# Kernel tuning notes

Hardware: AMD Instinct MI355X
Metric: run time of the kernel (lower is better)

Reference implementation:

```python
import jax, jax.numpy as jnp
import numpy as np
import math

HEAD_NUM = 16


def _split_qkv(qkv, head_num):
    # torch: rearrange(qkv, 'b t (d k h) -> k b h t d', k=3, h=head_num)
    B, T, E3 = qkv.shape
    d = E3 // (3 * head_num)
    qkv = qkv.reshape(B, T, d, 3, head_num)        # (b,t,d,k,h)
    qkv = jnp.transpose(qkv, (3, 0, 4, 1, 2))       # (k,b,h,t,d)
    return qkv[0], qkv[1], qkv[2]


def setup_inputs() -> dict:
    key = jax.random.key(0)
    ks = jax.random.split(key, 6)
    B, T, E = 4, 1024, 1024
    return {
        "x": jax.random.normal(ks[0], (B, T, E), dtype=jnp.float32),
        "y": jax.random.normal(ks[1], (B, T, E), dtype=jnp.float32),
        "Wqkv1": jax.random.normal(ks[2], (3 * E, E), dtype=jnp.float32) * 0.02,
        "Wqkv2": jax.random.normal(ks[3], (3 * E, E), dtype=jnp.float32) * 0.02,
        "Wout1": jax.random.normal(ks[4], (E, E), dtype=jnp.float32) * 0.02,
        "Wout2": jax.random.normal(ks[5], (E, E), dtype=jnp.float32) * 0.02,
    }


def reference(x, y, Wqkv1, Wqkv2, Wout1, Wout2):
    B, T, E = x.shape
    H = HEAD_NUM
    dk = math.sqrt(E / H)

    qkv1 = x @ Wqkv1.T                              # (B,T,3E)
    qkv2 = y @ Wqkv2.T
    q1, k1, v1 = _split_qkv(qkv1, H)                # each (B,H,T,d)
    q2, k2, v2 = _split_qkv(qkv2, H)

    # cross attention: stream-2 queries attend to stream-1 keys/values and vice versa
    energy1 = jnp.einsum('bhid,bhjd->bhij', q2, k1) / dk
    energy2 = jnp.einsum('bhid,bhjd->bhij', q1, k2) / dk
    attn1 = jax.nn.softmax(energy1, axis=-1)
    attn2 = jax.nn.softmax(energy2, axis=-1)

    xo = jnp.einsum('bhij,bhjd->bhid', attn1, v1)   # (B,H,T,d)
    yo = jnp.einsum('bhij,bhjd->bhid', attn2, v2)
    xo = jnp.transpose(xo, (0, 2, 1, 3)).reshape(B, T, E)  # b t (h d)
    yo = jnp.transpose(yo, (0, 2, 1, 3)).reshape(B, T, E)

    return xo @ Wout1.T, yo @ Wout2.T
```

## Files before the change

### kernel.cpp

```cpp
#include <hip/hip_runtime.h>
#include <hip/hip_bf16.h>

typedef __hip_bfloat16 bf16;
typedef __attribute__((ext_vector_type(8))) short short8;
typedef __attribute__((ext_vector_type(4))) short short4v;
typedef __attribute__((ext_vector_type(4))) float f32x4;

#define MFMA_BF16(a, b, c) __builtin_amdgcn_mfma_f32_16x16x32_bf16((a), (b), (c), 0, 0, 0)

#define QSCALE 0.1803368860111270f

__device__ __forceinline__ short f2bf(float f) {
    union { bf16 h; short s; } u;
    u.h = __float2bfloat16(f);
    return u.s;
}

#if defined(__has_builtin) && __has_builtin(__builtin_amdgcn_cvt_pk_bf16_f32)
typedef __attribute__((ext_vector_type(2))) __bf16 bf16x2_t;
__device__ __forceinline__ unsigned int pk2(float a, float b) {
    union { bf16x2_t v; unsigned int u; } x;
    x.v = __builtin_amdgcn_cvt_pk_bf16_f32(a, b);
    return x.u;
}
#else
__device__ __forceinline__ unsigned int pk2(float a, float b) {
    union { bf16 h[2]; unsigned int u; } x;
    x.h[0] = __float2bfloat16(a);
    x.h[1] = __float2bfloat16(b);
    return x.u;
}
#endif

__device__ __forceinline__ void gload16(const void* g, void* l) {
    __builtin_amdgcn_global_load_lds(
        (const __attribute__((address_space(1))) unsigned int*)g,
        (__attribute__((address_space(3))) unsigned int*)l, 16, 0, 0);
}

__global__ void cvt_fused(const float* __restrict__ x, const float* __restrict__ y,
                          const float* __restrict__ wo1, const float* __restrict__ wo2,
                          const float* __restrict__ wq1, const float* __restrict__ wq2,
                          bf16* __restrict__ ox, bf16* __restrict__ oy,
                          bf16* __restrict__ oo1, bf16* __restrict__ oo2,
                          bf16* __restrict__ oq1, bf16* __restrict__ oq2) {
    const int yb = blockIdx.y;
    if (yb < 4) {
        int i = blockIdx.x * 256 + threadIdx.x;
        const float* src; bf16* dst; int n4;
        switch (yb) {
            case 0:  src = x;   dst = ox;  n4 = 1048576; break;
            case 1:  src = y;   dst = oy;  n4 = 1048576; break;
            case 2:  src = wo1; dst = oo1; n4 = 262144;  break;
            default: src = wo2; dst = oo2; n4 = 262144;  break;
        }
        if (i >= n4) return;
        float4 f = reinterpret_cast<const float4*>(src)[i];
        short4v s;
        s.x = f2bf(f.x); s.y = f2bf(f.y); s.z = f2bf(f.z); s.w = f2bf(f.w);
        reinterpret_cast<short4v*>(dst)[i] = s;
    } else {
        const int np = blockIdx.x;
        if (np >= 3072) return;
        const int comp = np >> 10, rem = np & 1023, h = rem >> 6, d = rem & 63;
        const int srow = d * 48 + comp * 16 + h;
        const float* src = ((yb == 5) ? wq2 : wq1) + (long)srow * 1024;
        bf16* dst = ((yb == 5) ? oq2 : oq1) + (long)np * 1024;
        const float sc = (comp == 0) ? QSCALE : 1.0f;
        int t = threadIdx.x;
        float4 f = reinterpret_cast<const float4*>(src)[t];
        short4v s;
        s.x = f2bf(f.x * sc); s.y = f2bf(f.y * sc); s.z = f2bf(f.z * sc); s.w = f2bf(f.w * sc);
        reinterpret_cast<short4v*>(dst)[t] = s;
    }
}

template <int MODE>
__global__ __launch_bounds__(256)
void gemm_k(const bf16* __restrict__ A0g, const bf16* __restrict__ B0g,
            void* o0a, void* o0b, void* o0c,
            const bf16* __restrict__ A1g, const bf16* __restrict__ B1g,
            void* o1a, void* o1b, void* o1c, int N) {
    __shared__ short smem[20480];
    const int z = blockIdx.z;
    const short* A = reinterpret_cast<const short*>(z ? A1g : A0g);
    const short* B = reinterpret_cast<const short*>(z ? B1g : B0g);
    const int tid  = threadIdx.x;
    const int lane = tid & 63;
    const int w    = tid >> 6;
    const int wr   = w >> 1;
    const int wc   = w & 1;
    const int quad = lane >> 4;
    const int l16  = lane & 15;
    const long bM = (long)blockIdx.y * 128;

    f32x4 acc[4][4] = {};

    const int sr  = lane >> 2;
    const int scs = ((lane & 3) ^ (sr & 3)) * 8;
    const short* Ag0 = A + (bM + 32 * w + sr) * 1024 + scs;
    const short* Ag1 = Ag0 + 16 * 1024;
    const short* Bg0 = B + ((long)blockIdx.x * 128 + 32 * w + sr) * 1024 + scs;
    const short* Bg1 = Bg0 + 16 * 1024;

    const int sq = (quad ^ (l16 & 3)) * 8;

    {
        short* sb = smem;
        gload16(Ag0, sb + w * 1024);
        gload16(Ag1, sb + w * 1024 + 512);
        gload16(Bg0, sb + 4096 + w * 1024);
        gload16(Bg1, sb + 4096 + w * 1024 + 512);
    }
    __syncthreads();

    for (int iter = 0; iter < 32; ++iter) {
        const int cur = iter & 1;
        if (iter < 31) {
            const int koff = (iter + 1) * 32;
            short* sb = smem + (cur ^ 1) * 8192;
            gload16(Ag0 + koff, sb + w * 1024);
            gload16(Ag1 + koff, sb + w * 1024 + 512);
            gload16(Bg0 + koff, sb + 4096 + w * 1024);
            gload16(Bg1 + koff, sb + 4096 + w * 1024 + 512);
        }
        const short* Ab = smem + cur * 8192;
        const short* Bb = Ab + 4096;

        short8 af[4], bfr[4];
#pragma unroll
        for (int mt = 0; mt < 4; ++mt)
            af[mt] = *reinterpret_cast<const short8*>(&Ab[(wr * 64 + mt * 16 + l16) * 32 + sq]);
#pragma unroll
        for (int nt = 0; nt < 4; ++nt)
            bfr[nt] = *reinterpret_cast<const short8*>(&Bb[(wc * 64 + nt * 16 + l16) * 32 + sq]);
#pragma unroll
        for (int mt = 0; mt < 4; ++mt)
#pragma unroll
            for (int nt = 0; nt < 4; ++nt)
                acc[mt][nt] = MFMA_BF16(af[mt], bfr[nt], acc[mt][nt]);

        __syncthreads();
    }

    if (MODE == 1) {
        float* C = reinterpret_cast<float*>(z ? o1a : o0a);
        const long crow = bM + wr * 64 + quad * 4;
        const long ccol = (long)blockIdx.x * 128 + wc * 64 + l16;
#pragma unroll
        for (int mt = 0; mt < 4; ++mt)
#pragma unroll
            for (int nt = 0; nt < 4; ++nt)
#pragma unroll
                for (int r = 0; r < 4; ++r)
                    C[(crow + mt * 16 + r) * (long)N + ccol + nt * 16] = acc[mt][nt][r];
        return;
    }

    if (blockIdx.x < 16) {
        short* dst = reinterpret_cast<short*>(blockIdx.x >= 8 ? (z ? o1b : o0b)
                                                              : (z ? o1a : o0a));
        const int hd0 = (int)(blockIdx.x & 7) * 128 + wc * 64;
        const int b = (int)(bM >> 10);
        const int t0 = ((int)bM & 1023) + wr * 64 + quad * 4;
#pragma unroll
        for (int nt = 0; nt < 4; ++nt) {
            const int hd = hd0 + nt * 16 + l16;
            const int h = hd >> 6, d = hd & 63;
            short* dp = dst + ((long)(b * 16 + h) * 1024) * 64 + d;
#pragma unroll
            for (int mt = 0; mt < 4; ++mt)
#pragma unroll
                for (int r = 0; r < 4; ++r)
                    dp[(long)(t0 + mt * 16 + r) * 64] = f2bf(acc[mt][nt][r]);
        }
    } else {
        short* vT = reinterpret_cast<short*>(z ? o1c : o0c);
        const int h = ((int)blockIdx.x - 16) * 2 + wc;
        const int b = (int)(bM >> 10);
        const int tb = ((int)bM & 1023) + wr * 64;
        short* ws = smem + w * 4608;
#pragma unroll
        for (int nt = 0; nt < 4; ++nt)
#pragma unroll
            for (int mt = 0; mt < 4; ++mt) {
                uint2 uu;
                uu.x = pk2(acc[mt][nt][0], acc[mt][nt][1]);
                uu.y = pk2(acc[mt][nt][2], acc[mt][nt][3]);
                *reinterpret_cast<uint2*>(&ws[(nt * 16 + l16) * 72 + mt * 16 + quad * 4]) = uu;
            }
        short* vbase = vT + (long)(b * 16 + h) * 64 * 1024;
#pragma unroll
        for (int p = 0; p < 8; ++p) {
            const int d = p * 8 + (lane >> 3);
            const int ch = (lane & 7) * 8;
            short8 v = *reinterpret_cast<const short8*>(&ws[d * 72 + ch]);
            *reinterpret_cast<short8*>(&vbase[(long)d * 1024 + tb + ch]) = v;
        }
    }
}

__global__ __launch_bounds__(256)
void attn_kernel(const bf16* __restrict__ q0g, const bf16* __restrict__ k0g,
                 const bf16* __restrict__ v0g, bf16* __restrict__ o0g,
                 const bf16* __restrict__ q1g, const bf16* __restrict__ k1g,
                 const bf16* __restrict__ v1g, bf16* __restrict__ o1g) {
    __shared__ short smem[16384];
    const int bh = blockIdx.x;
    const int qt = blockIdx.y;
    const int z = blockIdx.z;
    const int b = bh >> 4, h = bh & 15;
    const int tid = threadIdx.x, lane = tid & 63, w = tid >> 6;
    const int quad = lane >> 4, l16 = lane & 15;

    const short* Qb = reinterpret_cast<const short*>(z ? q1g : q0g) + (long)bh * 1024 * 64;
    const short* Kb = reinterpret_cast<const short*>(z ? k1g : k0g) + (long)bh * 1024 * 64;
    const short* Vb = reinterpret_cast<const short*>(z ? v1g : v0g) + (long)bh * 64 * 1024;
    short* Ob = reinterpret_cast<short*>(z ? o1g : o0g);

    short8 qb[2][2];
#pragma unroll
    for (int qg = 0; qg < 2; ++qg) {
        const short* Qp = Qb + (long)(qt * 128 + qg * 64 + w * 16 + l16) * 64;
        qb[qg][0] = *reinterpret_cast<const short8*>(Qp + quad * 8);
        qb[qg][1] = *reinterpret_cast<const short8*>(Qp + 32 + quad * 8);
    }

    const int r8  = lane >> 3;
    const int sc8 = ((lane & 7) ^ r8) * 8;
    const short* Kg0 = Kb + (long)(16 * w + r8) * 64 + sc8;
    const short* Kg1 = Kg0 + 8 * 64;
    const short* Vg0 = Vb + (long)(16 * w + r8) * 1024 + sc8;
    const short* Vg1 = Vg0 + 8 * 1024;

    const int jbase = 8 * (l16 >> 2) + (l16 & 3);

    f32x4 o[2][4] = {};
    float li[2] = {0.f, 0.f};

    {
        short* sb = smem;
        gload16(Kg0, sb + w * 1024);
        gload16(Kg1, sb + w * 1024 + 512);
        gload16(Vg0, sb + 4096 + w * 1024);
        gload16(Vg1, sb + 4096 + w * 1024 + 512);
    }
    __syncthreads();

    for (int iter = 0; iter < 16; ++iter) {
        const int cur = iter & 1;
        if (iter < 15) {
            const long ko = (long)(iter + 1) * 4096;
            const long vo = (long)(iter + 1) * 64;
            short* sb = smem + (cur ^ 1) * 8192;
            gload16(Kg0 + ko, sb + w * 1024);
            gload16(Kg1 + ko, sb + w * 1024 + 512);
            gload16(Vg0 + vo, sb + 4096 + w * 1024);
            gload16(Vg1 + vo, sb + 4096 + w * 1024 + 512);
        }
        const short* Ks = smem + cur * 8192;
        const short* Vs = Ks + 4096;

        f32x4 st[2][4];
#pragma unroll
        for (int g = 0; g < 4; ++g) {
            const int goff = (g >> 1) * 32 + (g & 1) * 4;
            const int row = jbase + goff;
            const int s0 = (quad ^ (row & 7)) * 8;
            const short* kr = Ks + row * 64;
            short8 k0 = *reinterpret_cast<const short8*>(kr + s0);
            short8 k1 = *reinterpret_cast<const short8*>(kr + (s0 ^ 32));
#pragma unroll
            for (int qg = 0; qg < 2; ++qg) {
                f32x4 zf = {0.f, 0.f, 0.f, 0.f};
                zf = MFMA_BF16(k0, qb[qg][0], zf);
                zf = MFMA_BF16(k1, qb[qg][1], zf);
                st[qg][g] = zf;
            }
        }

        union { unsigned int u[4]; short8 s; } f0[2], f1[2];
#pragma unroll
        for (int qg = 0; qg < 2; ++qg) {
            float p[4][4];
            float rs = 0.f;
#pragma unroll
            for (int g = 0; g < 4; ++g)
#pragma unroll
                for (int r = 0; r < 4; ++r) {
                    float e = exp2f(st[qg][g][r]);
                    p[g][r] = e;
                    rs += e;
                }
            li[qg] += rs;
            f0[qg].u[0] = pk2(p[0][0], p[0][1]); f0[qg].u[1] = pk2(p[0][2], p[0][3]);
            f0[qg].u[2] = pk2(p[1][0], p[1][1]); f0[qg].u[3] = pk2(p[1][2], p[1][3]);
            f1[qg].u[0] = pk2(p[2][0], p[2][1]); f1[qg].u[1] = pk2(p[2][2], p[2][3]);
            f1[qg].u[2] = pk2(p[3][0], p[3][1]); f1[qg].u[3] = pk2(p[3][2], p[3][3]);
        }

#pragma unroll
        for (int dt = 0; dt < 4; ++dt) {
            const int rv = dt * 16 + l16;
            const int sv = (quad ^ (rv & 7)) * 8;
            const short* vr = Vs + rv * 64;
            short8 v0 = *reinterpret_cast<const short8*>(vr + sv);
            short8 v1 = *reinterpret_cast<const short8*>(vr + (sv ^ 32));
#pragma unroll
            for (int qg = 0; qg < 2; ++qg) {
                o[qg][dt] = MFMA_BF16(v0, f0[qg].s, o[qg][dt]);
                o[qg][dt] = MFMA_BF16(v1, f1[qg].s, o[qg][dt]);
            }
        }

        __syncthreads();
    }

#pragma unroll
    for (int qg = 0; qg < 2; ++qg) {
        li[qg] += __shfl_xor(li[qg], 16);
        li[qg] += __shfl_xor(li[qg], 32);
    }

#pragma unroll
    for (int qg = 0; qg < 2; ++qg) {
        short* Os = smem + qg * 5120 + w * 1280;
        const float rl = 1.0f / li[qg];
#pragma unroll
        for (int dt = 0; dt < 4; ++dt) {
            uint2 uu;
            uu.x = pk2(o[qg][dt][0] * rl, o[qg][dt][1] * rl);
            uu.y = pk2(o[qg][dt][2] * rl, o[qg][dt][3] * rl);
            *reinterpret_cast<uint2*>(&Os[l16 * 80 + dt * 16 + quad * 4]) = uu;
        }
#pragma unroll
        for (int p = 0; p < 2; ++p) {
            int row = p * 8 + (lane >> 3);
            int ch = (lane & 7) * 8;
            short8 v = *reinterpret_cast<const short8*>(&Os[row * 80 + ch]);
            *reinterpret_cast<short8*>(&Ob[((long)(b * 1024) + qt * 128 + qg * 64 + w * 16 + row) * 1024 + h * 64 + ch]) = v;
        }
    }
}

extern "C" void kernel_launch(void* const* d_in, const int* in_sizes, int n_in,
                              void* d_out, int out_size, void* d_ws, size_t ws_size,
                              hipStream_t stream) {
    const float* x     = (const float*)d_in[0];
    const float* y     = (const float*)d_in[1];
    const float* Wqkv1 = (const float*)d_in[2];
    const float* Wqkv2 = (const float*)d_in[3];
    const float* Wout1 = (const float*)d_in[4];
    const float* Wout2 = (const float*)d_in[5];

    char* ws = (char*)d_ws;
    bf16* Wqkv1b = (bf16*)(ws + 0);
    bf16* Wqkv2b = (bf16*)(ws + 6291456);
    bf16* Wout1b = (bf16*)(ws + 12582912);
    bf16* Wout2b = (bf16*)(ws + 14680064);
    bf16* xb     = (bf16*)(ws + 16777216);
    bf16* yb     = (bf16*)(ws + 25165824);
    bf16* q1     = (bf16*)(ws + 33554432);
    bf16* k1     = (bf16*)(ws + 41943040);
    bf16* v1T    = (bf16*)(ws + 50331648);
    bf16* q2     = (bf16*)(ws + 58720256);
    bf16* k2     = (bf16*)(ws + 67108864);
    bf16* v2T    = (bf16*)(ws + 75497472);
    bf16* xo     = xb;
    bf16* yo     = yb;

    cvt_fused<<<dim3(4096, 6), 256, 0, stream>>>(x, y, Wout1, Wout2, Wqkv1, Wqkv2,
                                                 xb, yb, Wout1b, Wout2b, Wqkv1b, Wqkv2b);

    gemm_k<0><<<dim3(24, 32, 2), 256, 0, stream>>>(xb, Wqkv1b, q1, k1, v1T,
                                                   yb, Wqkv2b, q2, k2, v2T, 3072);

    attn_kernel<<<dim3(64, 8, 2), 256, 0, stream>>>(q2, k1, v1T, xo,
                                                    q1, k2, v2T, yo);

    gemm_k<1><<<dim3(8, 32, 2), 256, 0, stream>>>(xo, Wout1b, (float*)d_out, nullptr, nullptr,
                                                  yo, Wout2b, ((float*)d_out) + 4194304, nullptr, nullptr,
                                                  1024);
}
```

Baseline: 264.2 us.

## Add 256x256 QKV GEMM with staged async loads and pipeline attention K/V loads

Replaces the 128x128 QKV projection GEMM with a 512-thread 256x256-tile kernel. It uses 128KB of dynamic LDS double-buffered across four sub-phases, vmcnt-gated barriers, and setprio around MFMA bursts to overlap global loads with compute. The attention kernel now splits K and V prefetches so V loads are issued after the QK MFMAs, and it waits on partial vmcnt instead of full syncthreads. It also changes the swizzle patterns. The aim is to raise data reuse per tile and hide load latency, at the cost of heavier register and LDS use that limits occupancy, plus hand-tuned waitcnt counts that are fragile.

After: 263.9 us. No clear change (-0.1%).

```diff
diff --git a/kernel.cpp b/kernel.cpp
--- a/kernel.cpp
+++ b/kernel.cpp
@@ -75,13 +75,168 @@
     }
 }
 
+#define GATE4 do { asm volatile("s_waitcnt vmcnt(4)" ::: "memory"); \
+    __builtin_amdgcn_s_barrier(); __builtin_amdgcn_sched_barrier(0); } while (0)
+
+__global__ __launch_bounds__(512, 2)
+void gemm_qkv256(const bf16* __restrict__ A0g, const bf16* __restrict__ B0g,
+                 void* o0a, void* o0b, void* o0c,
+                 const bf16* __restrict__ A1g, const bf16* __restrict__ B1g,
+                 void* o1a, void* o1b, void* o1c) {
+    extern __shared__ short smem[];
+    const int z = blockIdx.z;
+    const short* A = reinterpret_cast<const short*>(z ? A1g : A0g);
+    const short* B = reinterpret_cast<const short*>(z ? B1g : B0g);
+    const int tid  = threadIdx.x;
+    const int lane = tid & 63;
+    const int w    = tid >> 6;
+    const int quad = lane >> 4;
+    const int l16  = lane & 15;
+    const long M0 = (long)blockIdx.y * 256;
+    const long N0 = (long)blockIdx.x * 256;
+
+    const int rowblk = (w >> 2) * 64;
+    const int colblk = (w & 3) * 32;
+    const int cA0  = (quad ^ (l16 & 7)) * 8;
+    const int aoff = (rowblk + l16) * 64;
+    const int boff = 16384 + (colblk + l16) * 64;
+    const int w512 = w * 512;
+
+    const short* Asrc = A + (M0 + w * 8 + (lane >> 3)) * 1024 + ((lane & 7) ^ (lane >> 3)) * 8;
+    const short* Bsrc = B + (N0 + w * 8 + (lane >> 3)) * 1024 + ((lane & 7) ^ (lane >> 3)) * 8;
+
+    f32x4 acc[4][4][2] = {};
+    short8 af[4][2], bfv[2][2];
+
+#define SA256(half, tt, nbase) do { \
+    const short* _s = Asrc + (half) * 131072 + (tt) * 64; \
+    short* _d = smem + (nbase) + (half) * 8192 + w512; \
+    gload16(_s, _d); gload16(_s + 65536, _d + 4096); } while (0)
+#define SB256(half, tt, nbase) do { \
+    const short* _s = Bsrc + (half) * 131072 + (tt) * 64; \
+    short* _d = smem + (nbase) + 16384 + (half) * 8192 + w512; \
+    gload16(_s, _d); gload16(_s + 65536, _d + 4096); } while (0)
+#define RDA256(Ah, bbv) do { \
+    _Pragma("unroll") for (int mt = 0; mt < 4; ++mt) { \
+        const short* _p = &smem[(bbv) + (Ah) * 8192 + aoff + mt * 1024]; \
+        af[mt][0] = *reinterpret_cast<const short8*>(_p + cA0); \
+        af[mt][1] = *reinterpret_cast<const short8*>(_p + (cA0 ^ 32)); } } while (0)
+#define RDB256(Bh, bbv) do { \
+    _Pragma("unroll") for (int nt = 0; nt < 2; ++nt) { \
+        const short* _p = &smem[(bbv) + (Bh) * 8192 + boff + nt * 1024]; \
+        bfv[nt][0] = *reinterpret_cast<const short8*>(_p + cA0); \
+        bfv[nt][1] = *reinterpret_cast<const short8*>(_p + (cA0 ^ 32)); } } while (0)
+#define MM256(p) do { \
+    __builtin_amdgcn_s_setprio(1); \
+    _Pragma("unroll") for (int mt = 0; mt < 4; ++mt) \
+    _Pragma("unroll") for (int nt = 0; nt < 2; ++nt) { \
+        acc[p][mt][nt] = MFMA_BF16(af[mt][0], bfv[nt][0], acc[p][mt][nt]); \
+        acc[p][mt][nt] = MFMA_BF16(af[mt][1], bfv[nt][1], acc[p][mt][nt]); } \
+    __builtin_amdgcn_s_setprio(0); } while (0)
+
+    SA256(0, 0, 0); SB256(0, 0, 0); SB256(1, 0, 0); SA256(1, 0, 0);
+
+#pragma unroll 1
+    for (int t = 0; t < 15; ++t) {
+        const int bb = (t & 1) << 15;
+        const int nb = bb ^ 32768;
+        GATE4;
+        SA256(0, t + 1, nb);
+        RDA256(0, bb); RDB256(0, bb);
+        __builtin_amdgcn_sched_barrier(0);
+        MM256(0);
+        GATE4;
+        SB256(0, t + 1, nb);
+        RDB256(1, bb);
+        __builtin_amdgcn_sched_barrier(0);
+        MM256(1);
+        GATE4;
+        SB256(1, t + 1, nb);
+        RDA256(1, bb); RDB256(0, bb);
+        __builtin_amdgcn_sched_barrier(0);
+        MM256(2);
+        SA256(1, t + 1, nb);
+        RDB256(1, bb);
+        __builtin_amdgcn_sched_barrier(0);
+        MM256(3);
+    }
+    asm volatile("s_waitcnt vmcnt(0)" ::: "memory");
+    __builtin_amdgcn_s_barrier();
+    __builtin_amdgcn_sched_barrier(0);
+    {
+        const int bb = 32768;
+        RDA256(0, bb); RDB256(0, bb); MM256(0);
+        RDB256(1, bb); MM256(1);
+        RDA256(1, bb); RDB256(0, bb); MM256(2);
+        RDB256(1, bb); MM256(3);
+    }
+
+    if (blockIdx.x < 8) {
+        short* dst = reinterpret_cast<short*>(blockIdx.x < 4 ? (z ? o1a : o0a)
+                                                             : (z ? o1b : o0b));
+        const int b = (int)(M0 >> 10);
+        const int t00 = ((int)M0 & 1023);
+        const int hd00 = ((int)blockIdx.x & 3) * 256;
+#pragma unroll
+        for (int p = 0; p < 4; ++p) {
+            const int Ah = p >> 1, Bh = p & 1;
+            const int tr0 = t00 + Ah * 128 + rowblk + quad * 4;
+#pragma unroll
+            for (int nt = 0; nt < 2; ++nt) {
+                const int hd = hd00 + Bh * 128 + colblk + nt * 16 + l16;
+                const int h = hd >> 6, d = hd & 63;
+                short* dp = dst + (long)(b * 16 + h) * 65536 + d;
+#pragma unroll
+                for (int mt = 0; mt < 4; ++mt)
+#pragma unroll
+                    for (int r = 0; r < 4; ++r)
+                        dp[(long)(tr0 + mt * 16 + r) * 64] = f2bf(acc[p][mt][nt][r]);
+            }
+        }
+    } else {
+        short* vT = reinterpret_cast<short*>(z ? o1c : o0c);
+        const int b = (int)(M0 >> 10);
+        const int hd00 = ((int)blockIdx.x - 8) * 256;
+        short* ws = smem + w * 2304;
+        const int c8 = (lane & 7) * 8;
+        const int colr = lane >> 3;
+#pragma unroll
+        for (int p = 0; p < 4; ++p) {
+            const int Ah = p >> 1, Bh = p & 1;
+#pragma unroll
+            for (int nt = 0; nt < 2; ++nt)
+#pragma unroll
+                for (int mt = 0; mt < 4; ++mt) {
+                    uint2 uu;
+                    uu.x = pk2(acc[p][mt][nt][0], acc[p][mt][nt][1]);
+                    uu.y = pk2(acc[p][mt][nt][2], acc[p][mt][nt][3]);
+                    *reinterpret_cast<uint2*>(&ws[(nt * 16 + l16) * 72 + mt * 16 + quad * 4]) = uu;
+                }
+            const int tb = ((int)M0 & 1023) + Ah * 128 + rowblk + c8;
+#pragma unroll
+            for (int q4 = 0; q4 < 4; ++q4) {
+                const int col = q4 * 8 + colr;
+                const int hd = hd00 + Bh * 128 + colblk + col;
+                const int h = hd >> 6, d = hd & 63;
+                short8 v = *reinterpret_cast<const short8*>(&ws[col * 72 + c8]);
+                *reinterpret_cast<short8*>(&vT[(long)(b * 16 + h) * 65536 + (long)d * 1024 + tb]) = v;
+            }
+        }
+    }
+#undef SA256
+#undef SB256
+#undef RDA256
+#undef RDB256
+#undef MM256
+}
+
 template <int MODE>
 __global__ __launch_bounds__(256)
 void gemm_k(const bf16* __restrict__ A0g, const bf16* __restrict__ B0g,
             void* o0a, void* o0b, void* o0c,
             const bf16* __restrict__ A1g, const bf16* __restrict__ B1g,
             void* o1a, void* o1b, void* o1c, int N) {
-    __shared__ short smem[20480];
+    __shared__ short smem2[20480];
     const int z = blockIdx.z;
     const short* A = reinterpret_cast<const short*>(z ? A1g : A0g);
     const short* B = reinterpret_cast<const short*>(z ? B1g : B0g);
@@ -102,11 +257,10 @@
     const short* Ag1 = Ag0 + 16 * 1024;
     const short* Bg0 = B + ((long)blockIdx.x * 128 + 32 * w + sr) * 1024 + scs;
     const short* Bg1 = Bg0 + 16 * 1024;
-
     const int sq = (quad ^ (l16 & 3)) * 8;
 
     {
-        short* sb = smem;
+        short* sb = smem2;
         gload16(Ag0, sb + w * 1024);
         gload16(Ag1, sb + w * 1024 + 512);
         gload16(Bg0, sb + 4096 + w * 1024);
@@ -118,13 +272,13 @@
         const int cur = iter & 1;
         if (iter < 31) {
             const int koff = (iter + 1) * 32;
-            short* sb = smem + (cur ^ 1) * 8192;
+            short* sb = smem2 + (cur ^ 1) * 8192;
             gload16(Ag0 + koff, sb + w * 1024);
             gload16(Ag1 + koff, sb + w * 1024 + 512);
             gload16(Bg0 + koff, sb + 4096 + w * 1024);
             gload16(Bg1 + koff, sb + 4096 + w * 1024 + 512);
         }
-        const short* Ab = smem + cur * 8192;
+        const short* Ab = smem2 + cur * 8192;
         const short* Bb = Ab + 4096;
 
         short8 af[4], bfr[4];
@@ -156,7 +310,6 @@
                     C[(crow + mt * 16 + r) * (long)N + ccol + nt * 16] = acc[mt][nt][r];
         return;
     }
-
     if (blockIdx.x < 16) {
         short* dst = reinterpret_cast<short*>(blockIdx.x >= 8 ? (z ? o1b : o0b)
                                                               : (z ? o1a : o0a));
@@ -173,29 +326,6 @@
 #pragma unroll
                 for (int r = 0; r < 4; ++r)
                     dp[(long)(t0 + mt * 16 + r) * 64] = f2bf(acc[mt][nt][r]);
-        }
-    } else {
-        short* vT = reinterpret_cast<short*>(z ? o1c : o0c);
-        const int h = ((int)blockIdx.x - 16) * 2 + wc;
-        const int b = (int)(bM >> 10);
-        const int tb = ((int)bM & 1023) + wr * 64;
-        short* ws = smem + w * 4608;
-#pragma unroll
-        for (int nt = 0; nt < 4; ++nt)
-#pragma unroll
-            for (int mt = 0; mt < 4; ++mt) {
-                uint2 uu;
-                uu.x = pk2(acc[mt][nt][0], acc[mt][nt][1]);
-                uu.y = pk2(acc[mt][nt][2], acc[mt][nt][3]);
-                *reinterpret_cast<uint2*>(&ws[(nt * 16 + l16) * 72 + mt * 16 + quad * 4]) = uu;
-            }
-        short* vbase = vT + (long)(b * 16 + h) * 64 * 1024;
-#pragma unroll
-        for (int p = 0; p < 8; ++p) {
-            const int d = p * 8 + (lane >> 3);
-            const int ch = (lane & 7) * 8;
-            short8 v = *reinterpret_cast<const short8*>(&ws[d * 72 + ch]);
-            *reinterpret_cast<short8*>(&vbase[(long)d * 1024 + tb + ch]) = v;
         }
     }
 }
@@ -227,47 +357,48 @@
     }
 
     const int r8  = lane >> 3;
-    const int sc8 = ((lane & 7) ^ r8) * 8;
-    const short* Kg0 = Kb + (long)(16 * w + r8) * 64 + sc8;
-    const short* Kg1 = Kg0 + 8 * 64;
-    const short* Vg0 = Vb + (long)(16 * w + r8) * 1024 + sc8;
-    const short* Vg1 = Vg0 + 8 * 1024;
+    const int sc0 = ((lane & 7) ^ (r8 & 3)) * 8;
+    const short* Kg0 = Kb + (long)(16 * w + r8) * 64 + sc0;
+    const short* Kg1 = Kb + (long)(16 * w + 8 + r8) * 64 + (sc0 ^ 32);
+    const short* Vg0 = Vb + (long)(16 * w + r8) * 1024 + sc0;
+    const short* Vg1 = Vb + (long)(16 * w + 8 + r8) * 1024 + (sc0 ^ 32);
 
     const int jbase = 8 * (l16 >> 2) + (l16 & 3);
+    const int fKs = (l16 & 3) | (((l16 >> 2) & 1) << 2);
+    const int s0  = (quad ^ fKs) * 8;
+    const int fVs = (l16 & 3) | (((l16 >> 3) & 1) << 2);
+    const int sv  = (quad ^ fVs) * 8;
 
     f32x4 o[2][4] = {};
     float li[2] = {0.f, 0.f};
 
-    {
-        short* sb = smem;
-        gload16(Kg0, sb + w * 1024);
-        gload16(Kg1, sb + w * 1024 + 512);
-        gload16(Vg0, sb + 4096 + w * 1024);
-        gload16(Vg1, sb + 4096 + w * 1024 + 512);
-    }
-    __syncthreads();
-
+    gload16(Kg0, smem + w * 1024); gload16(Kg1, smem + w * 1024 + 512);
+    gload16(Vg0, smem + 4096 + w * 1024); gload16(Vg1, smem + 4096 + w * 1024 + 512);
+
+#pragma unroll 1
     for (int iter = 0; iter < 16; ++iter) {
         const int cur = iter & 1;
-        if (iter < 15) {
+        short* sb = smem + (cur ^ 1) * 8192;
+        const bool pre = iter < 15;
+        if (pre) {
             const long ko = (long)(iter + 1) * 4096;
-            const long vo = (long)(iter + 1) * 64;
-            short* sb = smem + (cur ^ 1) * 8192;
             gload16(Kg0 + ko, sb + w * 1024);
             gload16(Kg1 + ko, sb + w * 1024 + 512);
-            gload16(Vg0 + vo, sb + 4096 + w * 1024);
-            gload16(Vg1 + vo, sb + 4096 + w * 1024 + 512);
-        }
+        }
+        if (pre) { asm volatile("s_waitcnt vmcnt(4)" ::: "memory"); }
+        else     { asm volatile("s_waitcnt vmcnt(2)" ::: "memory"); }
+        __builtin_amdgcn_s_barrier();
+        __builtin_amdgcn_sched_barrier(0);
+
         const short* Ks = smem + cur * 8192;
         const short* Vs = Ks + 4096;
 
         f32x4 st[2][4];
+        __builtin_amdgcn_s_setprio(1);
 #pragma unroll
         for (int g = 0; g < 4; ++g) {
             const int goff = (g >> 1) * 32 + (g & 1) * 4;
-            const int row = jbase + goff;
-            const int s0 = (quad ^ (row & 7)) * 8;
-            const short* kr = Ks + row * 64;
+            const short* kr = Ks + (jbase + goff) * 64;
             short8 k0 = *reinterpret_cast<const short8*>(kr + s0);
             short8 k1 = *reinterpret_cast<const short8*>(kr + (s0 ^ 32));
 #pragma unroll
@@ -277,6 +408,13 @@
                 zf = MFMA_BF16(k1, qb[qg][1], zf);
                 st[qg][g] = zf;
             }
+        }
+        __builtin_amdgcn_s_setprio(0);
+
+        if (pre) {
+            const long vo = (long)(iter + 1) * 64;
+            gload16(Vg0 + vo, sb + 4096 + w * 1024);
+            gload16(Vg1 + vo, sb + 4096 + w * 1024 + 512);
         }
 
         union { unsigned int u[4]; short8 s; } f0[2], f1[2];
@@ -299,11 +437,15 @@
             f1[qg].u[2] = pk2(p[3][0], p[3][1]); f1[qg].u[3] = pk2(p[3][2], p[3][3]);
         }
 
+        if (pre) { asm volatile("s_waitcnt vmcnt(4)" ::: "memory"); }
+        else     { asm volatile("s_waitcnt vmcnt(0)" ::: "memory"); }
+        __builtin_amdgcn_s_barrier();
+        __builtin_amdgcn_sched_barrier(0);
+
+        __builtin_amdgcn_s_setprio(1);
 #pragma unroll
         for (int dt = 0; dt < 4; ++dt) {
-            const int rv = dt * 16 + l16;
-            const int sv = (quad ^ (rv & 7)) * 8;
-            const short* vr = Vs + rv * 64;
+            const short* vr = Vs + (dt * 16 + l16) * 64;
             short8 v0 = *reinterpret_cast<const short8*>(vr + sv);
             short8 v1 = *reinterpret_cast<const short8*>(vr + (sv ^ 32));
 #pragma unroll
@@ -312,9 +454,10 @@
                 o[qg][dt] = MFMA_BF16(v1, f1[qg].s, o[qg][dt]);
             }
         }
-
-        __syncthreads();
-    }
+        __builtin_amdgcn_s_setprio(0);
+    }
+
+    __syncthreads();
 
 #pragma unroll
     for (int qg = 0; qg < 2; ++qg) {
@@ -369,11 +512,18 @@
     bf16* xo     = xb;
     bf16* yo     = yb;
 
+    static bool s_attr = false;
+    if (!s_attr) {
+        (void)hipFuncSetAttribute(reinterpret_cast<const void*>(&gemm_qkv256),
+                                  hipFuncAttributeMaxDynamicSharedMemorySize, 131072);
+        s_attr = true;
+    }
+
     cvt_fused<<<dim3(4096, 6), 256, 0, stream>>>(x, y, Wout1, Wout2, Wqkv1, Wqkv2,
                                                  xb, yb, Wout1b, Wout2b, Wqkv1b, Wqkv2b);
 
-    gemm_k<0><<<dim3(24, 32, 2), 256, 0, stream>>>(xb, Wqkv1b, q1, k1, v1T,
-                                                   yb, Wqkv2b, q2, k2, v2T, 3072);
+    gemm_qkv256<<<dim3(12, 16, 2), 512, 131072, stream>>>(xb, Wqkv1b, q1, k1, v1T,
+                                                          yb, Wqkv2b, q2, k2, v2T);
 
     attn_kernel<<<dim3(64, 8, 2), 256, 0, stream>>>(q2, k1, v1T, xo,
                                                     q1, k2, v2T, yo);
```
